# Performance work log

Measured on AMD Instinct MI355X. Metric: run time of the kernel, lower is better.

The kernel has to match this reference:

```python
import jax, jax.numpy as jnp
import numpy as np

EPS = 1e-5  # BatchNorm eps (eval mode with running stats)

def conv1x1(x, w, b):
    # 1x1x1 Conv3d == channel matmul. x: (b,c,t,h,w), w: (o,c), b: (o,)
    return jnp.einsum('bcthw,oc->bothw', x, w) + b[None, :, None, None, None]

def pool122(x):
    # MaxPool3d kernel (1,2,2): max over non-overlapping 2x2 spatial windows
    b, c, t, h, w = x.shape
    return x.reshape(b, c, t, h // 2, 2, w // 2, 2).max(axis=(4, 6))

def setup_inputs() -> dict:
    key = jax.random.key(0)
    ks = jax.random.split(key, 13)
    C, Ci = 256, 128
    f32 = jnp.float32
    rn = lambda k, s, sc=1.0: jax.random.normal(k, s, dtype=f32) * sc
    return {
        'x': rn(ks[0], (4, C, 8, 32, 32)),
        'g_w': rn(ks[1], (Ci, C), 0.05), 'g_b': rn(ks[2], (Ci,), 0.05),
        'theta_w': rn(ks[3], (Ci, C), 0.05), 'theta_b': rn(ks[4], (Ci,), 0.05),
        'phi_w': rn(ks[5], (Ci, C), 0.05), 'phi_b': rn(ks[6], (Ci,), 0.05),
        'w_w': rn(ks[7], (C, Ci), 0.05), 'w_b': rn(ks[8], (C,), 0.05),
        'bn_gamma': rn(ks[9], (C,), 0.1) + 1.0,
        'bn_beta': rn(ks[10], (C,), 0.1),
        'bn_mean': rn(ks[11], (C,), 0.1),
        'bn_var': jax.random.uniform(ks[12], (C,), dtype=f32, minval=0.5, maxval=1.5),
    }

def reference(x, g_w, g_b, theta_w, theta_b, phi_w, phi_b, w_w, w_b,
              bn_gamma, bn_beta, bn_mean, bn_var):
    b = x.shape[0]
    ci = g_w.shape[0]
    # g, phi: conv then (1,2,2) maxpool (sub_sample=True)
    g_x = pool122(conv1x1(x, g_w, g_b)).reshape(b, ci, -1).transpose(0, 2, 1)      # (b, Nkv, ci)
    theta_x = conv1x1(x, theta_w, theta_b).reshape(b, ci, -1).transpose(0, 2, 1)   # (b, Nq, ci)
    phi_x = pool122(conv1x1(x, phi_w, phi_b)).reshape(b, ci, -1)                    # (b, ci, Nkv)
    f = jnp.einsum('bnc,bcm->bnm', theta_x, phi_x)                                  # (b, Nq, Nkv)
    attn = jax.nn.softmax(f, axis=-1)
    yy = jnp.einsum('bnm,bmc->bnc', attn, g_x)                                      # (b, Nq, ci)
    yy = yy.transpose(0, 2, 1).reshape(b, ci, *x.shape[2:])                         # (b, ci, t, h, w)
    wy = conv1x1(yy, w_w, w_b)
    # BatchNorm3d in eval mode with running stats
    scale = bn_gamma * jax.lax.rsqrt(bn_var + EPS)
    wy = wy * scale[None, :, None, None, None] + (bn_beta - bn_mean * scale)[None, :, None, None, None]
    return wy + x
```

## Files before the change

kernel.cpp:

```cpp
#include <hip/hip_runtime.h>
#include <hip/hip_bf16.h>

typedef __bf16 bf16x8 __attribute__((ext_vector_type(8)));
typedef __bf16 bf16x4 __attribute__((ext_vector_type(4)));
typedef __bf16 bf16x2 __attribute__((ext_vector_type(2)));
typedef float  f32x4  __attribute__((ext_vector_type(4)));

#define NB   4
#define C_   256
#define CI_  128
#define NSP  8192
#define NKV  2048
#define KVT  32
#define NT   (NKV/KVT)

__device__ __forceinline__ void gload_lds16(const void* g, void* l) {
    __builtin_amdgcn_global_load_lds(
        (const __attribute__((address_space(1))) void*)(unsigned long long)(uintptr_t)g,
        (__attribute__((address_space(3))) void*)(unsigned)(uintptr_t)l,
        16, 0, 0);
}

__global__ __launch_bounds__(256) void prep_kernel(
    const float* __restrict__ g_w,  const float* __restrict__ g_b,
    const float* __restrict__ th_w, const float* __restrict__ th_b,
    const float* __restrict__ ph_w, const float* __restrict__ ph_b,
    const float* __restrict__ w_w,  const float* __restrict__ w_b,
    const float* __restrict__ bn_g, const float* __restrict__ bn_be,
    const float* __restrict__ bn_m, const float* __restrict__ bn_v,
    __bf16* __restrict__ w_all, __bf16* __restrict__ w2,
    float* __restrict__ b_all, float* __restrict__ bnA, float* __restrict__ bnB)
{
    int idx = blockIdx.x * 256 + threadIdx.x;
    if (idx < 98304) {
        int o = idx >> 8, c = idx & 255;
        float v;
        if (o < 128)      v = th_w[o*256 + c];
        else if (o < 256) v = ph_w[(o-128)*256 + c];
        else              v = g_w[(o-256)*256 + c];
        w_all[idx] = (__bf16)v;
    } else if (idx < 131072) {
        int j = idx - 98304;
        w2[j] = (__bf16)w_w[j];
    } else if (idx < 131456) {
        int k = idx - 131072;
        float v;
        if (k < 128) v = th_b[k]; else if (k < 256) v = ph_b[k-128]; else v = g_b[k-256];
        b_all[k] = v;
    } else if (idx < 131712) {
        int m = idx - 131456;
        float sc = bn_g[m] * rsqrtf(bn_v[m] + 1e-5f);
        bnA[m] = sc;
        bnB[m] = w_b[m]*sc + bn_be[m] - bn_m[m]*sc;
    }
}

__global__ __launch_bounds__(256, 2) void proj_kernel(
    const float* __restrict__ x, const __bf16* __restrict__ w_all,
    const float* __restrict__ b_all,
    __bf16* __restrict__ Q, __bf16* __restrict__ K, __bf16* __restrict__ VT)
{
    const int b    = blockIdx.x >> 7;
    const int tile = blockIdx.x & 127;
    const int n0   = tile * 64;
    const int w    = threadIdx.x >> 6;
    const int lane = threadIdx.x & 63;
    const int lq   = lane & 15;
    const int g    = lane >> 4;

    const float* xb = x + b * (C_ * NSP);

    f32x4 acc[4][6];
    #pragma unroll
    for (int a = 0; a < 4; ++a)
        #pragma unroll
        for (int o = 0; o < 6; ++o) acc[a][o] = (f32x4){0.f,0.f,0.f,0.f};

    #pragma unroll 1
    for (int ck = 0; ck < 8; ++ck) {
        const int cbase = ck*32 + g*8;
        bf16x8 afr[4];
        #pragma unroll
        for (int nf = 0; nf < 4; ++nf) {
            const int n = n0 + nf*16 + lq;
            const float* xp = xb + cbase*NSP + n;
            bf16x8 v;
            #pragma unroll
            for (int e = 0; e < 8; ++e) v[e] = (__bf16)xp[e*NSP];
            afr[nf] = v;
        }
        #pragma unroll
        for (int oi = 0; oi < 6; ++oi) {
            const int orow = (w*6 + oi)*16 + lq;
            bf16x8 bfr = *(const bf16x8*)(w_all + orow*256 + cbase);
            #pragma unroll
            for (int nf = 0; nf < 4; ++nf)
                acc[nf][oi] = __builtin_amdgcn_mfma_f32_16x16x32_bf16(afr[nf], bfr, acc[nf][oi], 0,0,0);
        }
    }

    const int t  = n0 >> 10;
    const int h0 = (n0 & 1023) >> 5;
    const int kvrow0 = t*256 + (h0 >> 1)*16;

    #pragma unroll
    for (int oi = 0; oi < 6; ++oi) {
        const int ocol = (w*6 + oi)*16 + lq;
        const float bias = b_all[ocol];
        float v[4][4];
        #pragma unroll
        for (int nf = 0; nf < 4; ++nf)
            #pragma unroll
            for (int i = 0; i < 4; ++i) v[nf][i] = acc[nf][oi][i] + bias;

        const int seg = ocol >> 7;
        const int ol  = ocol & 127;
        if (seg == 0) {
            #pragma unroll
            for (int nf = 0; nf < 4; ++nf)
                #pragma unroll
                for (int i = 0; i < 4; ++i) {
                    int n = n0 + nf*16 + g*4 + i;
                    Q[(b*NSP + n)*CI_ + ol] = (__bf16)v[nf][i];
                }
        } else if (seg == 1) {
            #pragma unroll
            for (int nfp = 0; nfp < 2; ++nfp)
                #pragma unroll
                for (int j = 0; j < 2; ++j) {
                    float pv = fmaxf(fmaxf(v[nfp][2*j], v[nfp][2*j+1]),
                                     fmaxf(v[nfp+2][2*j], v[nfp+2][2*j+1]));
                    int wp = nfp*8 + g*2 + j;
                    K[(b*NKV + kvrow0 + wp)*CI_ + ol] = (__bf16)pv;
                }
        } else {
            #pragma unroll
            for (int nfp = 0; nfp < 2; ++nfp) {
                bf16x2 pk;
                #pragma unroll
                for (int j = 0; j < 2; ++j) {
                    float pv = fmaxf(fmaxf(v[nfp][2*j], v[nfp][2*j+1]),
                                     fmaxf(v[nfp+2][2*j], v[nfp+2][2*j+1]));
                    pk[j] = (__bf16)pv;
                }
                int wp = nfp*8 + g*2;
                *(bf16x2*)(VT + (b*CI_ + ol)*NKV + kvrow0 + wp) = pk;
            }
        }
    }
}

__global__ __launch_bounds__(256, 1) void attn_kernel(
    const __bf16* __restrict__ Q, const __bf16* __restrict__ K,
    const __bf16* __restrict__ VT, __bf16* __restrict__ yy)
{
    __shared__ __bf16 kbuf[3][32*128];
    __shared__ __bf16 vbuf[3][128*32];
    __shared__ __bf16 plds[4][32][40];

    const int b    = blockIdx.x >> 6;
    const int qt   = blockIdx.x & 63;
    const int w    = threadIdx.x >> 6;
    const int lane = threadIdx.x & 63;
    const int lq   = lane & 15;
    const int g    = lane >> 4;
    const int q0   = qt*128 + w*32;
    const float LOG2E = 1.4426950408889634f;

    bf16x8 qf[2][4];
    #pragma unroll
    for (int s = 0; s < 2; ++s) {
        const __bf16* qrow = Q + (size_t)(b*NSP + q0 + s*16 + lq)*CI_;
        #pragma unroll
        for (int kk = 0; kk < 4; ++kk) qf[s][kk] = *(const bf16x8*)(qrow + kk*32 + g*8);
    }

    float m_run[2] = {-1e30f, -1e30f}, l_run[2] = {0.f, 0.f};
    f32x4 oacc[2][8];
    #pragma unroll
    for (int s = 0; s < 2; ++s)
        #pragma unroll
        for (int d = 0; d < 8; ++d) oacc[s][d] = (f32x4){0.f,0.f,0.f,0.f};

    const __bf16* Kb0 = K  + (size_t)b*NKV*CI_;
    const __bf16* Vb0 = VT + (size_t)b*CI_*NKV;
    __bf16* pw = &plds[w][0][0];

    auto stage = [&](int bi, int kv0) {
        #pragma unroll
        for (int j = 0; j < 2; ++j) {
            int o   = w*2048 + j*1024 + lane*16;
            int row = o >> 8;
            int c   = (o & 255) ^ ((row & 7) << 4);
            const __bf16* src = Kb0 + (size_t)(kv0 + row)*CI_ + (c >> 1);
            gload_lds16(src, (char*)&kbuf[bi][0] + w*2048 + j*1024);
        }
        #pragma unroll
        for (int j = 0; j < 2; ++j) {
            int o    = w*2048 + j*1024 + lane*16;
            int row  = o >> 6;
            int slot = (o >> 4) & 3;
            int kc   = slot ^ ((row >> 1) & 3);
            const __bf16* src = Vb0 + (size_t)row*NKV + kv0 + kc*8;
            gload_lds16(src, (char*)&vbuf[bi][0] + w*2048 + j*1024);
        }
    };

    stage(0, 0);
    stage(1, KVT);

    for (int t = 0; t < NT; ++t) {
        asm volatile("s_waitcnt vmcnt(4)" ::: "memory");
        __builtin_amdgcn_s_barrier();
        __builtin_amdgcn_sched_barrier(0);

        {
            int tn = t + 2;
            int kvn = (tn < NT ? tn : NT-1) * KVT;
            stage(tn % 3, kvn);
        }

        const int bi = t % 3;
        const char* kb = (const char*)&kbuf[bi][0];
        const char* vb = (const char*)&vbuf[bi][0];

        f32x4 facc[2][2];
        #pragma unroll
        for (int s = 0; s < 2; ++s)
            #pragma unroll
            for (int nf = 0; nf < 2; ++nf) facc[s][nf] = (f32x4){0.f,0.f,0.f,0.f};
        __builtin_amdgcn_s_setprio(1);
        #pragma unroll
        for (int kk = 0; kk < 4; ++kk) {
            #pragma unroll
            for (int nf = 0; nf < 2; ++nf) {
                int row = nf*16 + lq;
                int c   = (kk*64 + g*16) ^ ((row & 7) << 4);
                bf16x8 kf = *(const bf16x8*)(kb + row*256 + c);
                facc[0][nf] = __builtin_amdgcn_mfma_f32_16x16x32_bf16(kf, qf[0][kk], facc[0][nf], 0,0,0);
                facc[1][nf] = __builtin_amdgcn_mfma_f32_16x16x32_bf16(kf, qf[1][kk], facc[1][nf], 0,0,0);
            }
        }
        __builtin_amdgcn_s_setprio(0);

        #pragma unroll
        for (int s = 0; s < 2; ++s) {
            float m0 = fmaxf(fmaxf(facc[s][0][0], facc[s][0][1]), fmaxf(facc[s][0][2], facc[s][0][3]));
            float m1 = fmaxf(fmaxf(facc[s][1][0], facc[s][1][1]), fmaxf(facc[s][1][2], facc[s][1][3]));
            float pmax = fmaxf(m0, m1);
            pmax = fmaxf(pmax, __shfl_xor(pmax, 16, 64));
            pmax = fmaxf(pmax, __shfl_xor(pmax, 32, 64));
            if (!__all(pmax - m_run[s] <= 8.f)) {
                float mnew = fmaxf(m_run[s], pmax);
                float corr = __builtin_amdgcn_exp2f((m_run[s] - mnew) * LOG2E);
                l_run[s] *= corr;
                #pragma unroll
                for (int d = 0; d < 8; ++d) {
                    oacc[s][d][0] *= corr; oacc[s][d][1] *= corr;
                    oacc[s][d][2] *= corr; oacc[s][d][3] *= corr;
                }
                m_run[s] = mnew;
            }
            float p[8];
            #pragma unroll
            for (int nf = 0; nf < 2; ++nf)
                #pragma unroll
                for (int i = 0; i < 4; ++i)
                    p[nf*4+i] = __builtin_amdgcn_exp2f((facc[s][nf][i] - m_run[s]) * LOG2E);
            float ps = ((p[0]+p[1]) + (p[2]+p[3])) + ((p[4]+p[5]) + (p[6]+p[7]));
            ps += __shfl_xor(ps, 16, 64);
            ps += __shfl_xor(ps, 32, 64);
            l_run[s] += ps;
            #pragma unroll
            for (int nf = 0; nf < 2; ++nf) {
                bf16x4 pk;
                #pragma unroll
                for (int i = 0; i < 4; ++i) pk[i] = (__bf16)p[nf*4+i];
                *(bf16x4*)(pw + (s*16 + lq)*40 + nf*16 + g*4) = pk;
            }
        }
        bf16x8 pb[2];
        #pragma unroll
        for (int s = 0; s < 2; ++s)
            pb[s] = *(const bf16x8*)(pw + (s*16 + lq)*40 + g*8);

        __builtin_amdgcn_s_setprio(1);
        #pragma unroll
        for (int df = 0; df < 8; ++df) {
            int row = df*16 + lq;
            int cb  = (g*16) ^ (((row >> 1) & 3) << 4);
            bf16x8 vf = *(const bf16x8*)(vb + row*64 + cb);
            oacc[0][df] = __builtin_amdgcn_mfma_f32_16x16x32_bf16(vf, pb[0], oacc[0][df], 0,0,0);
            oacc[1][df] = __builtin_amdgcn_mfma_f32_16x16x32_bf16(vf, pb[1], oacc[1][df], 0,0,0);
        }
        __builtin_amdgcn_s_setprio(0);
    }

    #pragma unroll
    for (int s = 0; s < 2; ++s) {
        float inv = 1.f / l_run[s];
        __bf16* yrow = yy + (size_t)(b*NSP + q0 + s*16 + lq)*CI_;
        #pragma unroll
        for (int df = 0; df < 8; ++df) {
            bf16x4 ov;
            #pragma unroll
            for (int i = 0; i < 4; ++i) ov[i] = (__bf16)(oacc[s][df][i] * inv);
            *(bf16x4*)(yrow + df*16 + g*4) = ov;
        }
    }
}

__global__ __launch_bounds__(256, 2) void out_kernel(
    const __bf16* __restrict__ yy, const __bf16* __restrict__ w2,
    const float* __restrict__ bnA, const float* __restrict__ bnB,
    const float* __restrict__ x, float* __restrict__ out)
{
    const int b    = blockIdx.x >> 7;
    const int tile = blockIdx.x & 127;
    const int n0   = tile * 64;
    const int w    = threadIdx.x >> 6;
    const int lane = threadIdx.x & 63;
    const int lq   = lane & 15;
    const int g    = lane >> 4;

    f32x4 acc[4][4];
    #pragma unroll
    for (int a = 0; a < 4; ++a)
        #pragma unroll
        for (int o = 0; o < 4; ++o) acc[a][o] = (f32x4){0.f,0.f,0.f,0.f};

    #pragma unroll
    for (int kk = 0; kk < 4; ++kk) {
        bf16x8 afr[4];
        #pragma unroll
        for (int nf = 0; nf < 4; ++nf)
            afr[nf] = *(const bf16x8*)(yy + (size_t)(b*NSP + n0 + nf*16 + lq)*CI_ + kk*32 + g*8);
        #pragma unroll
        for (int cf = 0; cf < 4; ++cf) {
            const int corow = (w*4 + cf)*16 + lq;
            bf16x8 bfr = *(const bf16x8*)(w2 + corow*CI_ + kk*32 + g*8);
            #pragma unroll
            for (int nf = 0; nf < 4; ++nf)
                acc[cf][nf] = __builtin_amdgcn_mfma_f32_16x16x32_bf16(afr[nf], bfr, acc[cf][nf], 0,0,0);
        }
    }

    #pragma unroll
    for (int cf = 0; cf < 4; ++cf) {
        const int co = (w*4 + cf)*16 + lq;
        const float A = bnA[co], Bv = bnB[co];
        #pragma unroll
        for (int nf = 0; nf < 4; ++nf) {
            const int n = n0 + nf*16 + g*4;
            size_t idx = (size_t)(b*C_ + co)*NSP + n;
            f32x4 xv = *(const f32x4*)(x + idx);
            f32x4 ov;
            #pragma unroll
            for (int i = 0; i < 4; ++i) ov[i] = acc[cf][nf][i]*A + Bv + xv[i];
            *(f32x4*)(out + idx) = ov;
        }
    }
}

extern "C" void kernel_launch(void* const* d_in, const int* in_sizes, int n_in,
                              void* d_out, int out_size, void* d_ws, size_t ws_size,
                              hipStream_t stream)
{
    const float* x    = (const float*)d_in[0];
    const float* g_w  = (const float*)d_in[1];
    const float* g_b  = (const float*)d_in[2];
    const float* th_w = (const float*)d_in[3];
    const float* th_b = (const float*)d_in[4];
    const float* ph_w = (const float*)d_in[5];
    const float* ph_b = (const float*)d_in[6];
    const float* w_w  = (const float*)d_in[7];
    const float* w_b  = (const float*)d_in[8];
    const float* bn_g = (const float*)d_in[9];
    const float* bn_be= (const float*)d_in[10];
    const float* bn_m = (const float*)d_in[11];
    const float* bn_v = (const float*)d_in[12];

    char* ws = (char*)d_ws;
    size_t off = 0;
    auto alloc = [&](size_t bytes) -> void* {
        void* p = ws + off;
        off += (bytes + 255) & ~(size_t)255;
        return p;
    };
    __bf16* w_all = (__bf16*)alloc(384*256*2);
    __bf16* w2    = (__bf16*)alloc(256*128*2);
    float*  b_all = (float*) alloc(384*4);
    float*  bnA   = (float*) alloc(256*4);
    float*  bnB   = (float*) alloc(256*4);
    __bf16* Qb    = (__bf16*)alloc((size_t)NB*NSP*CI_*2);
    __bf16* Kb    = (__bf16*)alloc((size_t)NB*NKV*CI_*2);
    __bf16* Vt    = (__bf16*)alloc((size_t)NB*CI_*NKV*2);
    __bf16* yyb   = (__bf16*)alloc((size_t)NB*NSP*CI_*2);

    prep_kernel<<<515, 256, 0, stream>>>(g_w, g_b, th_w, th_b, ph_w, ph_b, w_w, w_b,
                                         bn_g, bn_be, bn_m, bn_v,
                                         w_all, w2, b_all, bnA, bnB);
    proj_kernel<<<512, 256, 0, stream>>>(x, w_all, b_all, Qb, Kb, Vt);
    attn_kernel<<<256, 256, 0, stream>>>(Qb, Kb, Vt, yyb);
    out_kernel <<<512, 256, 0, stream>>>(yyb, w2, bnA, bnB, x, (float*)d_out);
}
```

Measured before the change: 218.8 us.

## Split attention KV range across two blocks and merge partials in output kernel

The attention kernel now splits the KV sequence into two halves, launching twice as many blocks (512 instead of 256) with occupancy hint 2, and writes unnormalized partial outputs plus running max/sum. The output projection kernel merges the two partials with log-sum-exp rescaling before its matmul. The projection kernel also moves to 512-thread blocks with fewer output tiles per wave. This aims to fill more CUs during attention (256 blocks underused the GPU), at the cost of extra partial-output memory traffic and merge arithmetic. Storing partials in bf16 before merging adds some rounding.

```diff
diff --git a/kernel.cpp b/kernel.cpp
--- a/kernel.cpp
+++ b/kernel.cpp
@@ -5,6 +5,7 @@
 typedef __bf16 bf16x4 __attribute__((ext_vector_type(4)));
 typedef __bf16 bf16x2 __attribute__((ext_vector_type(2)));
 typedef float  f32x4  __attribute__((ext_vector_type(4)));
+typedef float  f32x2  __attribute__((ext_vector_type(2)));
 
 #define NB   4
 #define C_   256
@@ -12,7 +13,8 @@
 #define NSP  8192
 #define NKV  2048
 #define KVT  32
-#define NT   (NKV/KVT)
+#define NTH  ((NKV/2)/KVT)
+#define NROW (NB*NSP)
 
 __device__ __forceinline__ void gload_lds16(const void* g, void* l) {
     __builtin_amdgcn_global_load_lds(
@@ -55,7 +57,7 @@
     }
 }
 
-__global__ __launch_bounds__(256, 2) void proj_kernel(
+__global__ __launch_bounds__(512, 2) void proj_kernel(
     const float* __restrict__ x, const __bf16* __restrict__ w_all,
     const float* __restrict__ b_all,
     __bf16* __restrict__ Q, __bf16* __restrict__ K, __bf16* __restrict__ VT)
@@ -70,11 +72,11 @@
 
     const float* xb = x + b * (C_ * NSP);
 
-    f32x4 acc[4][6];
+    f32x4 acc[4][3];
     #pragma unroll
     for (int a = 0; a < 4; ++a)
         #pragma unroll
-        for (int o = 0; o < 6; ++o) acc[a][o] = (f32x4){0.f,0.f,0.f,0.f};
+        for (int o = 0; o < 3; ++o) acc[a][o] = (f32x4){0.f,0.f,0.f,0.f};
 
     #pragma unroll 1
     for (int ck = 0; ck < 8; ++ck) {
@@ -90,8 +92,8 @@
             afr[nf] = v;
         }
         #pragma unroll
-        for (int oi = 0; oi < 6; ++oi) {
-            const int orow = (w*6 + oi)*16 + lq;
+        for (int oi = 0; oi < 3; ++oi) {
+            const int orow = (w*3 + oi)*16 + lq;
             bf16x8 bfr = *(const bf16x8*)(w_all + orow*256 + cbase);
             #pragma unroll
             for (int nf = 0; nf < 4; ++nf)
@@ -104,8 +106,8 @@
     const int kvrow0 = t*256 + (h0 >> 1)*16;
 
     #pragma unroll
-    for (int oi = 0; oi < 6; ++oi) {
-        const int ocol = (w*6 + oi)*16 + lq;
+    for (int oi = 0; oi < 3; ++oi) {
+        const int ocol = (w*3 + oi)*16 + lq;
         const float bias = b_all[ocol];
         float v[4][4];
         #pragma unroll
@@ -150,21 +152,25 @@
     }
 }
 
-__global__ __launch_bounds__(256, 1) void attn_kernel(
+__global__ __launch_bounds__(256, 2) void attn_kernel(
     const __bf16* __restrict__ Q, const __bf16* __restrict__ K,
-    const __bf16* __restrict__ VT, __bf16* __restrict__ yy)
+    const __bf16* __restrict__ VT, __bf16* __restrict__ o_part,
+    float* __restrict__ ml)
 {
     __shared__ __bf16 kbuf[3][32*128];
     __shared__ __bf16 vbuf[3][128*32];
     __shared__ __bf16 plds[4][32][40];
 
-    const int b    = blockIdx.x >> 6;
-    const int qt   = blockIdx.x & 63;
+    const int b    = blockIdx.x >> 7;
+    const int r    = blockIdx.x & 127;
+    const int qt   = r >> 1;
+    const int kvh  = r & 1;
     const int w    = threadIdx.x >> 6;
     const int lane = threadIdx.x & 63;
     const int lq   = lane & 15;
     const int g    = lane >> 4;
     const int q0   = qt*128 + w*32;
+    const int kvbase = kvh * (NKV/2);
     const float LOG2E = 1.4426950408889634f;
 
     bf16x8 qf[2][4];
@@ -206,17 +212,17 @@
         }
     };
 
-    stage(0, 0);
-    stage(1, KVT);
-
-    for (int t = 0; t < NT; ++t) {
+    stage(0, kvbase);
+    stage(1, kvbase + KVT);
+
+    for (int t = 0; t < NTH; ++t) {
         asm volatile("s_waitcnt vmcnt(4)" ::: "memory");
         __builtin_amdgcn_s_barrier();
         __builtin_amdgcn_sched_barrier(0);
 
         {
             int tn = t + 2;
-            int kvn = (tn < NT ? tn : NT-1) * KVT;
+            int kvn = kvbase + (tn < NTH ? tn : NTH-1) * KVT;
             stage(tn % 3, kvn);
         }
 
@@ -298,20 +304,25 @@
 
     #pragma unroll
     for (int s = 0; s < 2; ++s) {
-        float inv = 1.f / l_run[s];
-        __bf16* yrow = yy + (size_t)(b*NSP + q0 + s*16 + lq)*CI_;
+        const int row = b*NSP + q0 + s*16 + lq;
+        __bf16* orow = o_part + ((size_t)kvh*NROW + row)*CI_;
         #pragma unroll
         for (int df = 0; df < 8; ++df) {
             bf16x4 ov;
             #pragma unroll
-            for (int i = 0; i < 4; ++i) ov[i] = (__bf16)(oacc[s][df][i] * inv);
-            *(bf16x4*)(yrow + df*16 + g*4) = ov;
+            for (int i = 0; i < 4; ++i) ov[i] = (__bf16)oacc[s][df][i];
+            *(bf16x4*)(orow + df*16 + g*4) = ov;
+        }
+        if (g == 0) {
+            f32x2 v; v[0] = m_run[s]; v[1] = l_run[s];
+            *(f32x2*)(ml + ((size_t)kvh*NROW + row)*2) = v;
         }
     }
 }
 
 __global__ __launch_bounds__(256, 2) void out_kernel(
-    const __bf16* __restrict__ yy, const __bf16* __restrict__ w2,
+    const __bf16* __restrict__ o_part, const float* __restrict__ ml,
+    const __bf16* __restrict__ w2,
     const float* __restrict__ bnA, const float* __restrict__ bnB,
     const float* __restrict__ x, float* __restrict__ out)
 {
@@ -322,6 +333,21 @@
     const int lane = threadIdx.x & 63;
     const int lq   = lane & 15;
     const int g    = lane >> 4;
+    const float LOG2E = 1.4426950408889634f;
+
+    float c1[4], c2[4];
+    #pragma unroll
+    for (int nf = 0; nf < 4; ++nf) {
+        const size_t row = (size_t)b*NSP + n0 + nf*16 + lq;
+        f32x2 ml1 = *(const f32x2*)(ml + row*2);
+        f32x2 ml2 = *(const f32x2*)(ml + (NROW + row)*2);
+        float M  = fmaxf(ml1[0], ml2[0]);
+        float e1 = __builtin_amdgcn_exp2f((ml1[0] - M) * LOG2E);
+        float e2 = __builtin_amdgcn_exp2f((ml2[0] - M) * LOG2E);
+        float dinv = 1.f / (e1*ml1[1] + e2*ml2[1]);
+        c1[nf] = e1 * dinv;
+        c2[nf] = e2 * dinv;
+    }
 
     f32x4 acc[4][4];
     #pragma unroll
@@ -333,8 +359,16 @@
     for (int kk = 0; kk < 4; ++kk) {
         bf16x8 afr[4];
         #pragma unroll
-        for (int nf = 0; nf < 4; ++nf)
-            afr[nf] = *(const bf16x8*)(yy + (size_t)(b*NSP + n0 + nf*16 + lq)*CI_ + kk*32 + g*8);
+        for (int nf = 0; nf < 4; ++nf) {
+            const size_t off = ((size_t)b*NSP + n0 + nf*16 + lq)*CI_ + kk*32 + g*8;
+            bf16x8 o1 = *(const bf16x8*)(o_part + off);
+            bf16x8 o2 = *(const bf16x8*)(o_part + (size_t)NROW*CI_ + off);
+            bf16x8 af;
+            #pragma unroll
+            for (int e = 0; e < 8; ++e)
+                af[e] = (__bf16)(c1[nf]*(float)o1[e] + c2[nf]*(float)o2[e]);
+            afr[nf] = af;
+        }
         #pragma unroll
         for (int cf = 0; cf < 4; ++cf) {
             const int corow = (w*4 + cf)*16 + lq;
@@ -392,15 +426,16 @@
     float*  b_all = (float*) alloc(384*4);
     float*  bnA   = (float*) alloc(256*4);
     float*  bnB   = (float*) alloc(256*4);
-    __bf16* Qb    = (__bf16*)alloc((size_t)NB*NSP*CI_*2);
+    __bf16* Qb    = (__bf16*)alloc((size_t)NROW*CI_*2);
     __bf16* Kb    = (__bf16*)alloc((size_t)NB*NKV*CI_*2);
     __bf16* Vt    = (__bf16*)alloc((size_t)NB*CI_*NKV*2);
-    __bf16* yyb   = (__bf16*)alloc((size_t)NB*NSP*CI_*2);
+    __bf16* oPart = (__bf16*)alloc((size_t)2*NROW*CI_*2);
+    float*  mlB   = (float*) alloc((size_t)2*NROW*2*4);
 
     prep_kernel<<<515, 256, 0, stream>>>(g_w, g_b, th_w, th_b, ph_w, ph_b, w_w, w_b,
                                          bn_g, bn_be, bn_m, bn_v,
                                          w_all, w2, b_all, bnA, bnB);
-    proj_kernel<<<512, 256, 0, stream>>>(x, w_all, b_all, Qb, Kb, Vt);
-    attn_kernel<<<256, 256, 0, stream>>>(Qb, Kb, Vt, yyb);
-    out_kernel <<<512, 256, 0, stream>>>(yyb, w2, bnA, bnB, x, (float*)d_out);
-}
+    proj_kernel<<<512, 512, 0, stream>>>(x, w_all, b_all, Qb, Kb, Vt);
+    attn_kernel<<<512, 256, 0, stream>>>(Qb, Kb, Vt, oPart, mlB);
+    out_kernel <<<512, 256, 0, stream>>>(oPart, mlB, w2, bnA, bnB, x, (float*)d_out);
+}
```

New measurement: 196.0 us. -10.4%, faster.
